# Optimization experiments

Hardware: AMD Instinct MI355X
Metric: run time of the kernel (lower is better)

Reference implementation:

```python
import jax, jax.numpy as jnp
import numpy as np

N_NODES = 50000
N_EDGES = 800000
IN_DIM, HID_DIM, OUT_DIM = 128, 64, 64


def spmm(row, col, val, dense):
    # sparse [N,N] (COO) @ dense [N,D] -> [N,D]
    gathered = dense[col] * val[:, None]          # [E, D]
    return jax.ops.segment_sum(gathered, row, num_segments=N_NODES)


def setup_inputs() -> dict:
    key = jax.random.key(0)
    ks = jax.random.split(key, 8)
    stdv1 = 1.0 / np.sqrt(HID_DIM)
    stdv2 = 1.0 / np.sqrt(OUT_DIM)
    return {
        "x": jax.random.normal(ks[0], (N_NODES, IN_DIM), dtype=jnp.float32),
        "edge_row": jax.random.randint(ks[1], (N_EDGES,), 0, N_NODES, dtype=jnp.int32),
        "edge_col": jax.random.randint(ks[2], (N_EDGES,), 0, N_NODES, dtype=jnp.int32),
        "edge_val": jax.random.uniform(ks[3], (N_EDGES,), dtype=jnp.float32),
        "W1": jax.random.uniform(ks[4], (IN_DIM, HID_DIM), jnp.float32, -stdv1, stdv1),
        "b1": jax.random.uniform(ks[5], (HID_DIM,), jnp.float32, -stdv1, stdv1),
        "W2": jax.random.uniform(ks[6], (HID_DIM, OUT_DIM), jnp.float32, -stdv2, stdv2),
        "b2": jax.random.uniform(ks[7], (OUT_DIM,), jnp.float32, -stdv2, stdv2),
    }


def reference(x, edge_row, edge_col, edge_val, W1, b1, W2, b2):
    # layer 1: support = x @ W1; out = adj @ support + b1; relu
    h = jax.nn.relu(spmm(edge_row, edge_col, edge_val, x @ W1) + b1)
    # dropout: eval mode (training=False) -> identity
    # layer 2
    return spmm(edge_row, edge_col, edge_val, h @ W2) + b2
```

## Files before the change

### kernel.cpp

```cpp
#include <hip/hip_runtime.h>


#define N_NODES 50000
#define N_EDGES 800000
#define IN_DIM  128
#define HID_DIM 64
#define OUT_DIM 64

#define NB   196
#define EPB  4096
#define NBLK_E ((N_EDGES + EPB - 1) / EPB)
#define BCAP 5120
#define GEMM1_GRID ((N_NODES + 31) / 32)

typedef __attribute__((ext_vector_type(8))) short bf16x8;
typedef __attribute__((ext_vector_type(4))) float f32x4;

__device__ inline unsigned short f2bf(float x) {
    unsigned u = __float_as_uint(x);
    return (unsigned short)((u + 0x7FFFu + ((u >> 16) & 1u)) >> 16);
}
__device__ inline float bf2f(unsigned v) {
    return __uint_as_float(v << 16);
}

__global__ __launch_bounds__(256) void k_prep(
    const float* __restrict__ W1, unsigned short* __restrict__ Wt1,
    const float* __restrict__ W2, unsigned short* __restrict__ Wt2,
    int* __restrict__ bcur)
{
    int b = blockIdx.x, t = threadIdx.x;
    if (b < 32) {
        int e = b * 256 + t;
        int c = e / IN_DIM, k = e % IN_DIM;
        Wt1[c * IN_DIM + k] = f2bf(W1[k * HID_DIM + c]);
    } else if (b < 48) {
        int e2 = (b - 32) * 256 + t;
        int c = e2 / HID_DIM, k = e2 % HID_DIM;
        Wt2[c * HID_DIM + k] = f2bf(W2[k * OUT_DIM + c]);
    } else {
        if (t < NB) bcur[t] = 0;
    }
}

template <int K, bool IN_BF16>
__device__ __forceinline__ void gemm_body(
    unsigned short* __restrict__ Al, unsigned short* __restrict__ Bl,
    const void* __restrict__ Xv, const unsigned short* __restrict__ Wt,
    unsigned short* __restrict__ out, int bid, int t)
{
    int m0 = bid * 32;
    #pragma unroll
    for (int i = 0; i < K / 32; ++i) {
        int u4 = i * 256 + t;
        int col = (u4 * 8) / K, k = (u4 * 8) % K;
        uint4 w = ((const uint4*)Wt)[u4];
        int byte = (col * K + k) * 2;
        byte ^= ((col & 7) << 4);
        *(uint4*)((char*)Bl + byte) = w;
    }
    if (IN_BF16) {
        const unsigned short* X = (const unsigned short*)Xv;
        int row = t / (K / 8), k = (t % (K / 8)) * 8;
        int grow = m0 + row;
        uint4 v = make_uint4(0, 0, 0, 0);
        if (grow < N_NODES)
            v = *(const uint4*)(X + (size_t)grow * K + k);
        int byte = (row * K + k) * 2;
        byte ^= ((row & 7) << 4);
        *(uint4*)((char*)Al + byte) = v;
    } else {
        const float* X = (const float*)Xv;
        #pragma unroll
        for (int i = 0; i < K / 64; ++i) {
            int f8 = i * 256 + t;
            int row = (f8 * 8) / K, k = (f8 * 8) % K;
            int grow = m0 + row;
            float4 xa = make_float4(0.f, 0.f, 0.f, 0.f), xb = xa;
            if (grow < N_NODES) {
                const float4* src = (const float4*)(X + (size_t)grow * K + k);
                xa = src[0];
                xb = src[1];
            }
            uint4 v;
            v.x = (unsigned)f2bf(xa.x) | ((unsigned)f2bf(xa.y) << 16);
            v.y = (unsigned)f2bf(xa.z) | ((unsigned)f2bf(xa.w) << 16);
            v.z = (unsigned)f2bf(xb.x) | ((unsigned)f2bf(xb.y) << 16);
            v.w = (unsigned)f2bf(xb.z) | ((unsigned)f2bf(xb.w) << 16);
            int byte = (row * K + k) * 2;
            byte ^= ((row & 7) << 4);
            *(uint4*)((char*)Al + byte) = v;
        }
    }
    __syncthreads();

    int w = t >> 6, l = t & 63;
    int lr0 = (w & 1) * 16;
    int c0  = (w >> 1) * 32;
    int lrow = lr0 + (l & 15);
    int kb = (l >> 4) * 8;
    int col0 = c0 + (l & 15), col1 = col0 + 16;
    f32x4 acc0 = {0.f, 0.f, 0.f, 0.f}, acc1 = {0.f, 0.f, 0.f, 0.f};
    #pragma unroll
    for (int kc = 0; kc < K / 32; ++kc) {
        int ka = kc * 32 + kb;
        int ab = (lrow * K + ka) * 2;  ab ^= ((lrow & 7) << 4);
        int bb0 = (col0 * K + ka) * 2; bb0 ^= ((col0 & 7) << 4);
        int bb1 = (col1 * K + ka) * 2; bb1 ^= ((col1 & 7) << 4);
        bf16x8 a  = *(const bf16x8*)((const char*)Al + ab);
        bf16x8 b0 = *(const bf16x8*)((const char*)Bl + bb0);
        bf16x8 b1 = *(const bf16x8*)((const char*)Bl + bb1);
        acc0 = __builtin_amdgcn_mfma_f32_16x16x32_bf16(a, b0, acc0, 0, 0, 0);
        acc1 = __builtin_amdgcn_mfma_f32_16x16x32_bf16(a, b1, acc1, 0, 0, 0);
    }
    int grow0 = m0 + lr0 + (l >> 4) * 4;
    #pragma unroll
    for (int j = 0; j < 4; ++j) {
        int gr = grow0 + j;
        if (gr < N_NODES) {
            out[(size_t)gr * 64 + col0] = f2bf(acc0[j]);
            out[(size_t)gr * 64 + col1] = f2bf(acc1[j]);
        }
    }
}

__global__ __launch_bounds__(256) void k_mega1(
    const float* __restrict__ X, const unsigned short* __restrict__ Wt1,
    unsigned short* __restrict__ support,
    const int* __restrict__ erow, const int* __restrict__ ecol,
    const float* __restrict__ eval_, int* __restrict__ bcur,
    uint2* __restrict__ bucketed)
{
    __shared__ __align__(16) unsigned char smem[24576];
    int t = threadIdx.x;
    if (blockIdx.x < GEMM1_GRID) {
        gemm_body<IN_DIM, false>((unsigned short*)smem,
                                 (unsigned short*)(smem + 8192),
                                 X, Wt1, support, blockIdx.x, t);
        return;
    }
    int* lc    = (int*)smem;
    int* lbase = lc + NB;
    int blk = blockIdx.x - GEMM1_GRID;
    for (int i = t; i < NB; i += 256) lc[i] = 0;
    __syncthreads();
    int base = blk * EPB;
    int bkt[16], rnk[16];
    #pragma unroll 4
    for (int i = 0; i < 16; ++i) {
        int e = base + i * 256 + t;
        bkt[i] = -1;
        if (e < N_EDGES) {
            bkt[i] = erow[e] >> 8;
            rnk[i] = atomicAdd(&lc[bkt[i]], 1);
        }
    }
    __syncthreads();
    for (int i = t; i < NB; i += 256)
        lbase[i] = lc[i] ? atomicAdd(&bcur[i], lc[i]) : 0;
    __syncthreads();
    #pragma unroll 4
    for (int i = 0; i < 16; ++i) {
        int e = base + i * 256 + t;
        if (bkt[i] >= 0) {
            unsigned r = (unsigned)erow[e];
            unsigned w0 = (unsigned)ecol[e] | ((r & 255u) << 16);
            bucketed[(size_t)bkt[i] * BCAP + lbase[bkt[i]] + rnk[i]] =
                make_uint2(w0, __float_as_uint(eval_[e]));
        }
    }
}

__global__ __launch_bounds__(256) void k_bfinal(
    const int* __restrict__ bcur, const uint2* __restrict__ bucketed,
    uint2* __restrict__ pairs, int2* __restrict__ offs2)
{
    __shared__ uint2 ebuf[BCAP];
    __shared__ int rcnt[256];
    __shared__ int rsc[256];
    int t = threadIdx.x, b = blockIdx.x;
    int ne = bcur[b];
    int base0 = b * BCAP;
    rcnt[t] = 0;
    __syncthreads();
    for (int i = t; i < ne; i += 256) {
        uint2 p = bucketed[(size_t)base0 + i];
        ebuf[i] = p;
        atomicAdd(&rcnt[(p.x >> 16) & 255], 1);
    }
    __syncthreads();
    int v = rcnt[t];
    rsc[t] = v;
    __syncthreads();
    #pragma unroll
    for (int off = 1; off < 256; off <<= 1) {
        int add = (t >= off) ? rsc[t - off] : 0;
        __syncthreads();
        rsc[t] += add;
        __syncthreads();
    }
    int start = base0 + rsc[t] - v;
    int gr = (b << 8) + t;
    if (gr < N_NODES) offs2[gr] = make_int2(start, start + v);
    rcnt[t] = start;
    __syncthreads();
    for (int i = t; i < ne; i += 256) {
        uint2 p = ebuf[i];
        int pos = atomicAdd(&rcnt[(p.x >> 16) & 255], 1);
        pairs[pos] = make_uint2(p.x & 0xFFFFu, p.y);
    }
}

template <bool APPLY_RELU, bool OUT_BF16>
__global__ __launch_bounds__(256) void k_gather(
    const int2* __restrict__ offs2, const uint2* __restrict__ pairs,
    const unsigned short* __restrict__ dense, const float* __restrict__ bias,
    void* __restrict__ outp)
{
    int t = threadIdx.x;
    int r = __builtin_amdgcn_readfirstlane(blockIdx.x * 4 + (t >> 6));
    int d = t & 63;
    int2 oe = offs2[r];
    int e0 = oe.x, e1 = oe.y;
    float a[8];
    a[0] = bias[d];
    #pragma unroll
    for (int i = 1; i < 8; ++i) a[i] = 0.f;
    int e = e0;
    for (; e + 8 <= e1; e += 8) {
        uint2 p[8];
        #pragma unroll
        for (int i = 0; i < 8; ++i) p[i] = pairs[e + i];
        unsigned v[8];
        #pragma unroll
        for (int i = 0; i < 8; ++i) v[i] = dense[(size_t)p[i].x * 64u + d];
        #pragma unroll
        for (int i = 0; i < 8; ++i)
            a[i] = fmaf(__uint_as_float(p[i].y), bf2f(v[i]), a[i]);
    }
    if (e + 4 <= e1) {
        uint2 p[4];
        #pragma unroll
        for (int i = 0; i < 4; ++i) p[i] = pairs[e + i];
        unsigned v[4];
        #pragma unroll
        for (int i = 0; i < 4; ++i) v[i] = dense[(size_t)p[i].x * 64u + d];
        #pragma unroll
        for (int i = 0; i < 4; ++i)
            a[i] = fmaf(__uint_as_float(p[i].y), bf2f(v[i]), a[i]);
        e += 4;
    }
    for (; e < e1; ++e) {
        uint2 p = pairs[e];
        a[0] = fmaf(__uint_as_float(p.y),
                    bf2f(dense[(size_t)p.x * 64u + d]), a[0]);
    }
    float acc = ((a[0] + a[1]) + (a[2] + a[3])) +
                ((a[4] + a[5]) + (a[6] + a[7]));
    if (APPLY_RELU) acc = fmaxf(acc, 0.f);
    if (OUT_BF16)
        ((unsigned short*)outp)[(size_t)r * 64 + d] = f2bf(acc);
    else
        ((float*)outp)[(size_t)r * 64 + d] = acc;
}

__global__ __launch_bounds__(256) void k_gemm2(
    const unsigned short* __restrict__ X, const unsigned short* __restrict__ Wt,
    unsigned short* __restrict__ out)
{
    __shared__ unsigned short Al[32 * HID_DIM];
    __shared__ unsigned short Bl[64 * HID_DIM];
    gemm_body<HID_DIM, true>(Al, Bl, X, Wt, out, blockIdx.x, threadIdx.x);
}

extern "C" void kernel_launch(void* const* d_in, const int* in_sizes, int n_in,
                              void* d_out, int out_size, void* d_ws, size_t ws_size,
                              hipStream_t stream)
{
    const float* x     = (const float*)d_in[0];
    const int*   erow  = (const int*)d_in[1];
    const int*   ecol  = (const int*)d_in[2];
    const float* eval_ = (const float*)d_in[3];
    const float* W1    = (const float*)d_in[4];
    const float* b1    = (const float*)d_in[5];
    const float* W2    = (const float*)d_in[6];
    const float* b2    = (const float*)d_in[7];
    float* out = (float*)d_out;

    uint2* pairs    = (uint2*)d_ws;
    uint2* bucketed = pairs + (size_t)NB * BCAP;
    unsigned short* support = (unsigned short*)(bucketed + (size_t)NB * BCAP);
    unsigned short* agg1 = support + (size_t)N_NODES * 64;
    unsigned short* Wt1 = agg1 + (size_t)N_NODES * 64;
    unsigned short* Wt2 = Wt1 + IN_DIM * HID_DIM;
    int*  bcur  = (int*)(Wt2 + HID_DIM * OUT_DIM);
    int2* offs2 = (int2*)(bcur + NB + 2);

    const int row_grid = N_NODES / 4;

    k_prep<<<49, 256, 0, stream>>>(W1, Wt1, W2, Wt2, bcur);
    k_mega1<<<GEMM1_GRID + NBLK_E, 256, 0, stream>>>(
        x, Wt1, support, erow, ecol, eval_, bcur, bucketed);
    k_bfinal<<<NB, 256, 0, stream>>>(bcur, bucketed, pairs, offs2);
    k_gather<true, true><<<row_grid, 256, 0, stream>>>(
        offs2, pairs, support, b1, agg1);
    k_gemm2<<<GEMM1_GRID, 256, 0, stream>>>(agg1, Wt2, support);
    k_gather<false, false><<<row_grid, 256, 0, stream>>>(
        offs2, pairs, support, b2, out);
}
```

Measured before the change: 94.95 us.

## Split dense features into column halves and rebucket edges by 64 rows

Stores the support and hidden activations as two 32-column halves. Each gather kernel now runs two passes over the rows, one per half, with two edges handled per wave step, so the gathered working set per pass is half as large and more likely to stay in L2. Edge bucketing moves from 256-row to 64-row buckets with smaller edge blocks, and the per-bucket prefix scan becomes a single-wave shuffle scan. The cost is twice as many gather blocks, a cross-lane reduction at the end, and each edge index list being read twice.

Measured after the change: 150.0 us. 58.0% more time.

```diff
diff --git a/kernel.cpp b/kernel.cpp
--- a/kernel.cpp
+++ b/kernel.cpp
@@ -7,11 +7,14 @@
 #define HID_DIM 64
 #define OUT_DIM 64
 
-#define NB   196
-#define EPB  4096
+#define RB   64
+#define NB   ((N_NODES + RB - 1) / RB)
+#define EPB  1024
 #define NBLK_E ((N_EDGES + EPB - 1) / EPB)
-#define BCAP 5120
+#define BCAP 1280
 #define GEMM1_GRID ((N_NODES + 31) / 32)
+#define GRID_HALF (N_NODES / 4)
+#define HALF_ELEMS ((size_t)N_NODES * 32)
 
 typedef __attribute__((ext_vector_type(8))) short bf16x8;
 typedef __attribute__((ext_vector_type(4))) float f32x4;
@@ -39,7 +42,7 @@
         int c = e2 / HID_DIM, k = e2 % HID_DIM;
         Wt2[c * HID_DIM + k] = f2bf(W2[k * OUT_DIM + c]);
     } else {
-        if (t < NB) bcur[t] = 0;
+        for (int i = t; i < NB; i += 256) bcur[i] = 0;
     }
 }
 
@@ -63,9 +66,11 @@
         const unsigned short* X = (const unsigned short*)Xv;
         int row = t / (K / 8), k = (t % (K / 8)) * 8;
         int grow = m0 + row;
+        int hf = k >> 5;
         uint4 v = make_uint4(0, 0, 0, 0);
         if (grow < N_NODES)
-            v = *(const uint4*)(X + (size_t)grow * K + k);
+            v = *(const uint4*)(X + (size_t)hf * HALF_ELEMS
+                                + (size_t)grow * 32 + (k & 31));
         int byte = (row * K + k) * 2;
         byte ^= ((row & 7) << 4);
         *(uint4*)((char*)Al + byte) = v;
@@ -113,13 +118,15 @@
         acc0 = __builtin_amdgcn_mfma_f32_16x16x32_bf16(a, b0, acc0, 0, 0, 0);
         acc1 = __builtin_amdgcn_mfma_f32_16x16x32_bf16(a, b1, acc1, 0, 0, 0);
     }
+    unsigned short* oh = out + (size_t)(w >> 1) * HALF_ELEMS;
+    int lc0 = l & 15;
     int grow0 = m0 + lr0 + (l >> 4) * 4;
     #pragma unroll
     for (int j = 0; j < 4; ++j) {
         int gr = grow0 + j;
         if (gr < N_NODES) {
-            out[(size_t)gr * 64 + col0] = f2bf(acc0[j]);
-            out[(size_t)gr * 64 + col1] = f2bf(acc1[j]);
+            oh[(size_t)gr * 32 + lc0]      = f2bf(acc0[j]);
+            oh[(size_t)gr * 32 + lc0 + 16] = f2bf(acc1[j]);
         }
     }
 }
@@ -145,13 +152,13 @@
     for (int i = t; i < NB; i += 256) lc[i] = 0;
     __syncthreads();
     int base = blk * EPB;
-    int bkt[16], rnk[16];
-    #pragma unroll 4
-    for (int i = 0; i < 16; ++i) {
+    int bkt[4], rnk[4];
+    #pragma unroll
+    for (int i = 0; i < 4; ++i) {
         int e = base + i * 256 + t;
         bkt[i] = -1;
         if (e < N_EDGES) {
-            bkt[i] = erow[e] >> 8;
+            bkt[i] = erow[e] >> 6;
             rnk[i] = atomicAdd(&lc[bkt[i]], 1);
         }
     }
@@ -159,12 +166,12 @@
     for (int i = t; i < NB; i += 256)
         lbase[i] = lc[i] ? atomicAdd(&bcur[i], lc[i]) : 0;
     __syncthreads();
-    #pragma unroll 4
-    for (int i = 0; i < 16; ++i) {
+    #pragma unroll
+    for (int i = 0; i < 4; ++i) {
         int e = base + i * 256 + t;
         if (bkt[i] >= 0) {
             unsigned r = (unsigned)erow[e];
-            unsigned w0 = (unsigned)ecol[e] | ((r & 255u) << 16);
+            unsigned w0 = (unsigned)ecol[e] | ((r & 63u) << 16);
             bucketed[(size_t)bkt[i] * BCAP + lbase[bkt[i]] + rnk[i]] =
                 make_uint2(w0, __float_as_uint(eval_[e]));
         }
@@ -176,37 +183,36 @@
     uint2* __restrict__ pairs, int2* __restrict__ offs2)
 {
     __shared__ uint2 ebuf[BCAP];
-    __shared__ int rcnt[256];
-    __shared__ int rsc[256];
+    __shared__ int rcnt[RB];
+    __shared__ int rcur[RB];
     int t = threadIdx.x, b = blockIdx.x;
     int ne = bcur[b];
     int base0 = b * BCAP;
-    rcnt[t] = 0;
+    if (t < RB) rcnt[t] = 0;
     __syncthreads();
     for (int i = t; i < ne; i += 256) {
         uint2 p = bucketed[(size_t)base0 + i];
         ebuf[i] = p;
-        atomicAdd(&rcnt[(p.x >> 16) & 255], 1);
-    }
-    __syncthreads();
-    int v = rcnt[t];
-    rsc[t] = v;
-    __syncthreads();
-    #pragma unroll
-    for (int off = 1; off < 256; off <<= 1) {
-        int add = (t >= off) ? rsc[t - off] : 0;
-        __syncthreads();
-        rsc[t] += add;
-        __syncthreads();
-    }
-    int start = base0 + rsc[t] - v;
-    int gr = (b << 8) + t;
-    if (gr < N_NODES) offs2[gr] = make_int2(start, start + v);
-    rcnt[t] = start;
+        atomicAdd(&rcnt[(p.x >> 16) & 63], 1);
+    }
+    __syncthreads();
+    if (t < RB) {
+        int v = rcnt[t];
+        int s = v;
+        #pragma unroll
+        for (int off = 1; off < RB; off <<= 1) {
+            int o = __shfl_up(s, off, 64);
+            if (t >= off) s += o;
+        }
+        int start = base0 + s - v;
+        int gr = b * RB + t;
+        if (gr < N_NODES) offs2[gr] = make_int2(start, start + v);
+        rcur[t] = start;
+    }
     __syncthreads();
     for (int i = t; i < ne; i += 256) {
         uint2 p = ebuf[i];
-        int pos = atomicAdd(&rcnt[(p.x >> 16) & 255], 1);
+        int pos = atomicAdd(&rcur[(p.x >> 16) & 63], 1);
         pairs[pos] = make_uint2(p.x & 0xFFFFu, p.y);
     }
 }
@@ -218,50 +224,48 @@
     void* __restrict__ outp)
 {
     int t = threadIdx.x;
-    int r = __builtin_amdgcn_readfirstlane(blockIdx.x * 4 + (t >> 6));
-    int d = t & 63;
+    int half = (blockIdx.x >= GRID_HALF) ? 1 : 0;
+    int rb = blockIdx.x - half * GRID_HALF;
+    int r = __builtin_amdgcn_readfirstlane(rb * 4 + (t >> 6));
+    int l = t & 63;
+    int sub = l >> 5, d = l & 31;
+    const unsigned short* dh = dense + (size_t)half * HALF_ELEMS;
     int2 oe = offs2[r];
     int e0 = oe.x, e1 = oe.y;
-    float a[8];
-    a[0] = bias[d];
-    #pragma unroll
-    for (int i = 1; i < 8; ++i) a[i] = 0.f;
+    float a[4];
+    a[0] = (sub == 0) ? bias[half * 32 + d] : 0.f;
+    a[1] = a[2] = a[3] = 0.f;
     int e = e0;
     for (; e + 8 <= e1; e += 8) {
-        uint2 p[8];
-        #pragma unroll
-        for (int i = 0; i < 8; ++i) p[i] = pairs[e + i];
-        unsigned v[8];
-        #pragma unroll
-        for (int i = 0; i < 8; ++i) v[i] = dense[(size_t)p[i].x * 64u + d];
-        #pragma unroll
-        for (int i = 0; i < 8; ++i)
-            a[i] = fmaf(__uint_as_float(p[i].y), bf2f(v[i]), a[i]);
-    }
-    if (e + 4 <= e1) {
         uint2 p[4];
         #pragma unroll
-        for (int i = 0; i < 4; ++i) p[i] = pairs[e + i];
+        for (int i = 0; i < 4; ++i) p[i] = pairs[e + 2 * i + sub];
         unsigned v[4];
         #pragma unroll
-        for (int i = 0; i < 4; ++i) v[i] = dense[(size_t)p[i].x * 64u + d];
+        for (int i = 0; i < 4; ++i)
+            v[i] = dh[(size_t)(p[i].x & 0xFFFFu) * 32u + d];
         #pragma unroll
         for (int i = 0; i < 4; ++i)
             a[i] = fmaf(__uint_as_float(p[i].y), bf2f(v[i]), a[i]);
-        e += 4;
-    }
-    for (; e < e1; ++e) {
-        uint2 p = pairs[e];
-        a[0] = fmaf(__uint_as_float(p.y),
-                    bf2f(dense[(size_t)p.x * 64u + d]), a[0]);
-    }
-    float acc = ((a[0] + a[1]) + (a[2] + a[3])) +
-                ((a[4] + a[5]) + (a[6] + a[7]));
-    if (APPLY_RELU) acc = fmaxf(acc, 0.f);
-    if (OUT_BF16)
-        ((unsigned short*)outp)[(size_t)r * 64 + d] = f2bf(acc);
-    else
-        ((float*)outp)[(size_t)r * 64 + d] = acc;
+    }
+    for (; e < e1; e += 2) {
+        int idx = e + sub;
+        if (idx < e1) {
+            uint2 p = pairs[idx];
+            a[0] = fmaf(__uint_as_float(p.y),
+                        bf2f(dh[(size_t)(p.x & 0xFFFFu) * 32u + d]), a[0]);
+        }
+    }
+    float s = (a[0] + a[1]) + (a[2] + a[3]);
+    s += __shfl_xor(s, 32, 64);
+    if (APPLY_RELU) s = fmaxf(s, 0.f);
+    if (sub == 0) {
+        if (OUT_BF16)
+            ((unsigned short*)outp)[(size_t)half * HALF_ELEMS
+                                    + (size_t)r * 32 + d] = f2bf(s);
+        else
+            ((float*)outp)[(size_t)r * 64 + half * 32 + d] = s;
+    }
 }
 
 __global__ __launch_bounds__(256) void k_gemm2(
@@ -290,21 +294,19 @@
     uint2* pairs    = (uint2*)d_ws;
     uint2* bucketed = pairs + (size_t)NB * BCAP;
     unsigned short* support = (unsigned short*)(bucketed + (size_t)NB * BCAP);
-    unsigned short* agg1 = support + (size_t)N_NODES * 64;
-    unsigned short* Wt1 = agg1 + (size_t)N_NODES * 64;
+    unsigned short* agg1 = support + 2 * HALF_ELEMS;
+    unsigned short* Wt1 = agg1 + 2 * HALF_ELEMS;
     unsigned short* Wt2 = Wt1 + IN_DIM * HID_DIM;
     int*  bcur  = (int*)(Wt2 + HID_DIM * OUT_DIM);
     int2* offs2 = (int2*)(bcur + NB + 2);
-
-    const int row_grid = N_NODES / 4;
 
     k_prep<<<49, 256, 0, stream>>>(W1, Wt1, W2, Wt2, bcur);
     k_mega1<<<GEMM1_GRID + NBLK_E, 256, 0, stream>>>(
         x, Wt1, support, erow, ecol, eval_, bcur, bucketed);
     k_bfinal<<<NB, 256, 0, stream>>>(bcur, bucketed, pairs, offs2);
-    k_gather<true, true><<<row_grid, 256, 0, stream>>>(
+    k_gather<true, true><<<2 * GRID_HALF, 256, 0, stream>>>(
         offs2, pairs, support, b1, agg1);
     k_gemm2<<<GEMM1_GRID, 256, 0, stream>>>(agg1, Wt2, support);
-    k_gather<false, false><<<row_grid, 256, 0, stream>>>(
+    k_gather<false, false><<<2 * GRID_HALF, 256, 0, stream>>>(
         offs2, pairs, support, b2, out);
 }
```

## Use finer row buckets and smaller edge blocks in the CSR build

Applied to the files above, without the earlier changes.

Row buckets shrink from 256 to 64 rows, so there are 782 buckets instead of 196, and each edge block covers 1024 edges instead of 4096. The bucket finalize kernel now runs its 64-row prefix scan with wavefront shuffles instead of a shared-memory scan that needed a barrier on every step. The goal is more blocks in both the bucketing and finalize stages, and less barrier overhead in the scan. In exchange there are more global atomics on the bucket counters, each edge block does more per-bucket work, and a bucket can hold at most 1280 edges. That cap leaves less headroom for unusually large buckets.

Result: slower. 100.8 us (+6.1%).

```diff
diff --git a/kernel.cpp b/kernel.cpp
--- a/kernel.cpp
+++ b/kernel.cpp
@@ -7,10 +7,11 @@
 #define HID_DIM 64
 #define OUT_DIM 64
 
-#define NB   196
-#define EPB  4096
+#define RB   64
+#define NB   ((N_NODES + RB - 1) / RB)
+#define EPB  1024
 #define NBLK_E ((N_EDGES + EPB - 1) / EPB)
-#define BCAP 5120
+#define BCAP 1280
 #define GEMM1_GRID ((N_NODES + 31) / 32)
 
 typedef __attribute__((ext_vector_type(8))) short bf16x8;
@@ -39,7 +40,7 @@
         int c = e2 / HID_DIM, k = e2 % HID_DIM;
         Wt2[c * HID_DIM + k] = f2bf(W2[k * OUT_DIM + c]);
     } else {
-        if (t < NB) bcur[t] = 0;
+        for (int i = t; i < NB; i += 256) bcur[i] = 0;
     }
 }
 
@@ -145,13 +146,13 @@
     for (int i = t; i < NB; i += 256) lc[i] = 0;
     __syncthreads();
     int base = blk * EPB;
-    int bkt[16], rnk[16];
-    #pragma unroll 4
-    for (int i = 0; i < 16; ++i) {
+    int bkt[4], rnk[4];
+    #pragma unroll
+    for (int i = 0; i < 4; ++i) {
         int e = base + i * 256 + t;
         bkt[i] = -1;
         if (e < N_EDGES) {
-            bkt[i] = erow[e] >> 8;
+            bkt[i] = erow[e] >> 6;
             rnk[i] = atomicAdd(&lc[bkt[i]], 1);
         }
     }
@@ -159,12 +160,12 @@
     for (int i = t; i < NB; i += 256)
         lbase[i] = lc[i] ? atomicAdd(&bcur[i], lc[i]) : 0;
     __syncthreads();
-    #pragma unroll 4
-    for (int i = 0; i < 16; ++i) {
+    #pragma unroll
+    for (int i = 0; i < 4; ++i) {
         int e = base + i * 256 + t;
         if (bkt[i] >= 0) {
             unsigned r = (unsigned)erow[e];
-            unsigned w0 = (unsigned)ecol[e] | ((r & 255u) << 16);
+            unsigned w0 = (unsigned)ecol[e] | ((r & 63u) << 16);
             bucketed[(size_t)bkt[i] * BCAP + lbase[bkt[i]] + rnk[i]] =
                 make_uint2(w0, __float_as_uint(eval_[e]));
         }
@@ -176,37 +177,36 @@
     uint2* __restrict__ pairs, int2* __restrict__ offs2)
 {
     __shared__ uint2 ebuf[BCAP];
-    __shared__ int rcnt[256];
-    __shared__ int rsc[256];
+    __shared__ int rcnt[RB];
+    __shared__ int rcur[RB];
     int t = threadIdx.x, b = blockIdx.x;
     int ne = bcur[b];
     int base0 = b * BCAP;
-    rcnt[t] = 0;
+    if (t < RB) rcnt[t] = 0;
     __syncthreads();
     for (int i = t; i < ne; i += 256) {
         uint2 p = bucketed[(size_t)base0 + i];
         ebuf[i] = p;
-        atomicAdd(&rcnt[(p.x >> 16) & 255], 1);
-    }
-    __syncthreads();
-    int v = rcnt[t];
-    rsc[t] = v;
-    __syncthreads();
-    #pragma unroll
-    for (int off = 1; off < 256; off <<= 1) {
-        int add = (t >= off) ? rsc[t - off] : 0;
-        __syncthreads();
-        rsc[t] += add;
-        __syncthreads();
-    }
-    int start = base0 + rsc[t] - v;
-    int gr = (b << 8) + t;
-    if (gr < N_NODES) offs2[gr] = make_int2(start, start + v);
-    rcnt[t] = start;
+        atomicAdd(&rcnt[(p.x >> 16) & 63], 1);
+    }
+    __syncthreads();
+    if (t < RB) {
+        int v = rcnt[t];
+        int s = v;
+        #pragma unroll
+        for (int off = 1; off < RB; off <<= 1) {
+            int o = __shfl_up(s, off, 64);
+            if (t >= off) s += o;
+        }
+        int start = base0 + s - v;
+        int gr = b * RB + t;
+        if (gr < N_NODES) offs2[gr] = make_int2(start, start + v);
+        rcur[t] = start;
+    }
     __syncthreads();
     for (int i = t; i < ne; i += 256) {
         uint2 p = ebuf[i];
-        int pos = atomicAdd(&rcnt[(p.x >> 16) & 255], 1);
+        int pos = atomicAdd(&rcur[(p.x >> 16) & 63], 1);
         pairs[pos] = make_uint2(p.x & 0xFFFFu, p.y);
     }
 }
@@ -294,7 +294,7 @@
     unsigned short* Wt1 = agg1 + (size_t)N_NODES * 64;
     unsigned short* Wt2 = Wt1 + IN_DIM * HID_DIM;
     int*  bcur  = (int*)(Wt2 + HID_DIM * OUT_DIM);
-    int2* offs2 = (int2*)(bcur + NB + 2);
+    int2* offs2 = (int2*)(bcur + NB);
 
     const int row_grid = N_NODES / 4;
 
```

## Stage bucketed edges in shared memory to coalesce bucket scatter writes

Applied to the files above, without the earlier changes.

The edge-bucketing blocks now keep each edge's packed col/row/value in registers, compute a block-local exclusive scan of the per-bucket counts, and write the edges sorted by bucket into a shared buffer. A second pass then writes contiguous runs to global bucket storage, so the global writes are grouped by bucket instead of scattered per edge. The bucket id is packed into the top bits of the first word for the second pass. This adds a shared-memory scan with many barriers and raises LDS use from 24KB to about 35KB, which may reduce occupancy for the GEMM blocks that share this kernel. The offs2 offset also changes.

After: 96.24 us. Within noise of the previous version (+1.4%).

```diff
diff --git a/kernel.cpp b/kernel.cpp
--- a/kernel.cpp
+++ b/kernel.cpp
@@ -7,7 +7,8 @@
 #define HID_DIM 64
 #define OUT_DIM 64
 
-#define NB   196
+#define RB   256
+#define NB   ((N_NODES + RB - 1) / RB)
 #define EPB  4096
 #define NBLK_E ((N_EDGES + EPB - 1) / EPB)
 #define BCAP 5120
@@ -131,7 +132,7 @@
     const float* __restrict__ eval_, int* __restrict__ bcur,
     uint2* __restrict__ bucketed)
 {
-    __shared__ __align__(16) unsigned char smem[24576];
+    __shared__ __align__(16) unsigned char smem[35392];
     int t = threadIdx.x;
     if (blockIdx.x < GEMM1_GRID) {
         gemm_body<IN_DIM, false>((unsigned short*)smem,
@@ -139,34 +140,58 @@
                                  X, Wt1, support, blockIdx.x, t);
         return;
     }
-    int* lc    = (int*)smem;
-    int* lbase = lc + NB;
+    uint2* sbuf  = (uint2*)smem;
+    int*   lc    = (int*)(smem + 32768);
+    int*   scr   = (int*)(smem + 33568);
+    int*   lbase = (int*)(smem + 34592);
     int blk = blockIdx.x - GEMM1_GRID;
-    for (int i = t; i < NB; i += 256) lc[i] = 0;
+    if (t < NB) lc[t] = 0;
     __syncthreads();
     int base = blk * EPB;
+    int ne_total = min(EPB, N_EDGES - base);
     int bkt[16], rnk[16];
+    unsigned w0v[16], vv[16];
     #pragma unroll 4
     for (int i = 0; i < 16; ++i) {
         int e = base + i * 256 + t;
         bkt[i] = -1;
         if (e < N_EDGES) {
-            bkt[i] = erow[e] >> 8;
+            unsigned r = (unsigned)erow[e];
+            bkt[i] = (int)(r >> 8);
+            w0v[i] = (unsigned)ecol[e] | ((r & 255u) << 16)
+                     | ((unsigned)(r >> 8) << 24);
+            vv[i] = __float_as_uint(eval_[e]);
             rnk[i] = atomicAdd(&lc[bkt[i]], 1);
         }
     }
     __syncthreads();
-    for (int i = t; i < NB; i += 256)
-        lbase[i] = lc[i] ? atomicAdd(&bcur[i], lc[i]) : 0;
+    int cnt = (t < NB) ? lc[t] : 0;
+    scr[t] = cnt;
+    __syncthreads();
+    #pragma unroll
+    for (int off = 1; off < 256; off <<= 1) {
+        int add = (t >= off) ? scr[t - off] : 0;
+        __syncthreads();
+        scr[t] += add;
+        __syncthreads();
+    }
+    int excl = scr[t] - cnt;
+    __syncthreads();
+    scr[t] = excl;
+    if (t < NB) lbase[t] = cnt ? atomicAdd(&bcur[t], cnt) : 0;
+    __syncthreads();
+    #pragma unroll 4
+    for (int i = 0; i < 16; ++i)
+        if (bkt[i] >= 0)
+            sbuf[scr[bkt[i]] + rnk[i]] = make_uint2(w0v[i], vv[i]);
     __syncthreads();
     #pragma unroll 4
     for (int i = 0; i < 16; ++i) {
-        int e = base + i * 256 + t;
-        if (bkt[i] >= 0) {
-            unsigned r = (unsigned)erow[e];
-            unsigned w0 = (unsigned)ecol[e] | ((r & 255u) << 16);
-            bucketed[(size_t)bkt[i] * BCAP + lbase[bkt[i]] + rnk[i]] =
-                make_uint2(w0, __float_as_uint(eval_[e]));
+        int idx = i * 256 + t;
+        if (idx < ne_total) {
+            uint2 p = sbuf[idx];
+            int bk = (int)(p.x >> 24);
+            bucketed[(size_t)bk * BCAP + lbase[bk] + (idx - scr[bk])] = p;
         }
     }
 }
@@ -294,7 +319,7 @@
     unsigned short* Wt1 = agg1 + (size_t)N_NODES * 64;
     unsigned short* Wt2 = Wt1 + IN_DIM * HID_DIM;
     int*  bcur  = (int*)(Wt2 + HID_DIM * OUT_DIM);
-    int2* offs2 = (int2*)(bcur + NB + 2);
+    int2* offs2 = (int2*)(bcur + NB);
 
     const int row_grid = N_NODES / 4;
 
```
